# Kernel tuning notes

Hardware: AMD Instinct MI355X
Metric: run time of the kernel (lower is better)

## Reference

```python
import jax, jax.numpy as jnp
import numpy as np

# --- basis bookkeeping (mirrors TwoBodyToSpherical._generate_buffers) ---
METADATA = np.array([3, 2, 1], dtype=np.int64)          # shells per l
N_IRREPS = 2 * np.arange(3, dtype=np.int64) + 1          # 2l+1
REP_OFFSETS = np.concatenate([[0], np.cumsum(METADATA * N_IRREPS)[:-1]])
NUM_REPS_1D = int((METADATA * N_IRREPS).sum())           # = 14
M_IDX_MAP = {0: [0], 1: [0, 2, 1], 2: [0, 1, 2, 3, 4]}
ANGULAR = {"s": 0, "p": 1, "d": 2}

C_AOS = ["1s", "2s", "3s"] + ["2p"] * 3 + ["3p"] * 3 + ["3d"] * 5
H_AOS = ["1s", "2s"]


def _build_repid_map(aos):
    # faithful port of the per-element repid_map construction (valence_only=True)
    repid = np.zeros(len(aos), dtype=np.int64)
    dst_n, l_last, m_qc = 0, 0, 0
    for i, ao in enumerate(aos):
        l = ANGULAR[ao[1]]
        if l > l_last:
            dst_n = 0
        repid[i] = REP_OFFSETS[l] + dst_n + M_IDX_MAP[l][m_qc] * METADATA[l]
        if m_qc == 2 * l:
            m_qc = 0
            dst_n += 1
        else:
            m_qc += 1
        l_last = l
    return repid


def setup_inputs() -> dict:
    key = jax.random.key(0)
    maps = {"C": _build_repid_map(C_AOS), "H": _build_repid_map(H_AOS)}
    atomsybs = ["C"] * 400 + ["H"] * 100               # 500 atoms
    n_atoms = len(atomsybs)
    dst_rep_ids_1d = np.concatenate([maps[a] for a in atomsybs])
    lens = np.array([len(maps[a]) for a in atomsybs], dtype=np.int64)
    dst_offsets_1d = np.repeat(np.arange(n_atoms, dtype=np.int64), lens)
    dst_flat_ids_1d = dst_offsets_1d * NUM_REPS_1D + dst_rep_ids_1d  # [N_ao]=5800
    n_ao = dst_flat_ids_1d.shape[0]
    feat_ten = jax.random.normal(key, (n_ao, n_ao), dtype=jnp.float32)
    return {
        "feat_ten": feat_ten,
        "dst_flat_ids_1d": jnp.asarray(dst_flat_ids_1d, dtype=jnp.int32),
        "n_atoms": n_atoms,
        "num_reps_1d": NUM_REPS_1D,
    }


def reference(feat_ten, dst_flat_ids_1d, n_atoms, num_reps_1d):
    total = n_atoms * num_reps_1d                        # 7000
    # 2D destination flat ids: outer-sum of 1D ids (rep_dims=(0,1))
    ids2d = (dst_flat_ids_1d[:, None] * total + dst_flat_ids_1d[None, :]).reshape(-1)
    flat = feat_ten.reshape(-1)
    out_flat = jnp.zeros((total * total,), dtype=feat_ten.dtype).at[ids2d].add(flat)
    # view(n_atoms, R, n_atoms, R) then transpose(1,2) -> [A, A, R, R]
    out = out_flat.reshape(n_atoms, num_reps_1d, n_atoms, num_reps_1d)
    return jnp.transpose(out, (0, 2, 1, 3))
```

## Files before the change

kernel.cpp:

```cpp
#include <hip/hip_runtime.h>

constexpr int R = 14;
constexpr int A = 500;
constexpr int TOTAL = A * R;
constexpr int TILE = R * R;
constexpr int G = 25;
constexpr int NG = A / G;
constexpr int SUPER = 4;
constexpr int NSUP = NG / SUPER;
constexpr int WP = 356;
constexpr int CHUNK = G * TILE;

__global__ __launch_bounds__(1024) void setup_kernel(
        const int* __restrict__ dst, int n_ao,
        int* __restrict__ inv, int* __restrict__ arow,
        int* __restrict__ ncols, int* __restrict__ pm) {
    int tid = threadIdx.x;
    for (int t = tid; t < TOTAL; t += 1024) inv[t] = -1;
    __syncthreads();
    for (int t = tid; t < n_ao; t += 1024) inv[dst[t]] = t;
    __syncthreads();
    if (tid < A) {
        int a = tid, lo = 0x7fffffff, hi = -1;
#pragma unroll
        for (int r = 0; r < R; ++r) {
            int v = inv[a * R + r];
            if (v >= 0) { lo = min(lo, v); hi = max(hi, v); }
        }
        arow[a] = lo;
        ncols[a] = hi - lo + 1;
#pragma unroll
        for (int r = 0; r < R; ++r) {
            int v = inv[a * R + r];
            pm[a * R + r] = (v >= 0) ? (v - lo) : -1;
        }
    }
}

__global__ __launch_bounds__(512, 6) void tile_kernel(
        const float* __restrict__ feat,
        const int* __restrict__ arow,
        const int* __restrict__ ncols,
        const int* __restrict__ pm,
        float* __restrict__ out, int n_ao) {
    const int gs  = blockIdx.x % NSUP;
    const int a1  = blockIdx.x / NSUP;
    const int tid = threadIdx.x;

    __shared__ float buf[2][R][WP];
    __shared__ int s_pr[R];
    __shared__ int s_pc[SUPER][G * R];
    __shared__ int s_off[SUPER][G];
    __shared__ int s_colA[SUPER];
    __shared__ int s_W4[SUPER];

    const int arow1 = arow[a1];
    const int n1    = ncols[a1];
    const int gbase = gs * (SUPER * G);

    if (tid < R) s_pr[tid] = pm[a1 * R + tid];
    for (int t = tid; t < SUPER * G * R; t += 512)
        (&s_pc[0][0])[t] = pm[gbase * R + t];
    if (tid < SUPER) {
        const int g0 = gbase + tid * G;
        const int colA = arow[g0] & ~3;
        s_colA[tid] = colA;
        s_W4[tid]   = (arow[g0 + G - 1] + ncols[g0 + G - 1] - colA + 3) >> 2;
    }
    if (tid < SUPER * G) {
        const int sI = tid / G, i = tid - sI * G;
        const int g0 = gbase + sI * G;
        s_off[sI][i] = arow[g0 + i] - (arow[g0] & ~3);
    }
    __syncthreads();

    int a2i_[3], dk_[3][4], ci_[3][4];
    bool val_[3];
#pragma unroll
    for (int j = 0; j < 3; ++j) {
        const int o4 = tid * 4 + j * 2048;
        val_[j] = (o4 < CHUNK);
        const int o = val_[j] ? o4 : 0;
        int a2i = o / TILE;
        int e   = o - a2i * TILE;
        int r1  = e / R;
        int r2  = e - r1 * R;
        a2i_[j] = a2i;
#pragma unroll
        for (int k = 0; k < 4; ++k) {
            dk_[j][k] = s_pr[r1];
            ci_[j][k] = a2i * R + r2;
            if (++r2 == R) { r2 = 0; ++r1; }
        }
    }

    const int d0  = tid >> 7;
    const int c4  = tid & 127;
    const int rs4 = n_ao >> 2;
    const float4* feat4 = reinterpret_cast<const float4*>(feat);

    float4 rg[4];

    auto stage_load = [&](int s) {
        const int W4 = s_W4[s];
        if (c4 < W4) {
            const float4* src = feat4 + (long long)arow1 * rs4 + (s_colA[s] >> 2) + c4;
#pragma unroll
            for (int u = 0; u < 4; ++u) {
                const int d = d0 + u * 4;
                if (d < n1) rg[u] = src[(long long)d * rs4];
            }
        }
    };
    auto stage_write = [&](int nb, int s) {
        const int W4 = s_W4[s];
        if (c4 < W4) {
#pragma unroll
            for (int u = 0; u < 4; ++u) {
                const int d = d0 + u * 4;
                if (d < n1)
                    *reinterpret_cast<float4*>(&buf[nb][d][c4 << 2]) = rg[u];
            }
        }
    };

    stage_load(0);
    stage_write(0, 0);
    __syncthreads();

    int cb = 0;
    for (int s = 0; s < SUPER; ++s) {
        if (s + 1 < SUPER) stage_load(s + 1);

        const long long outbase =
            ((long long)a1 * A + gbase + s * G) * (long long)TILE;
        const int* pcS = &s_pc[s][0];
#pragma unroll
        for (int j = 0; j < 3; ++j) {
            if (!val_[j]) continue;
            const int off = s_off[s][a2i_[j]];
            float4 v;
            float* vp = &v.x;
#pragma unroll
            for (int k = 0; k < 4; ++k) {
                const int d = dk_[j][k];
                const int c = pcS[ci_[j][k]];
                vp[k] = ((d | c) >= 0) ? buf[cb][d][off + c] : 0.0f;
            }
            *reinterpret_cast<float4*>(out + outbase + tid * 4 + j * 2048) = v;
        }

        if (s + 1 < SUPER) {
            stage_write(cb ^ 1, s + 1);
            __syncthreads();
            cb ^= 1;
        }
    }
}

extern "C" void kernel_launch(void* const* d_in, const int* in_sizes, int n_in,
                              void* d_out, int out_size, void* d_ws, size_t ws_size,
                              hipStream_t stream) {
    const float* feat = (const float*)d_in[0];
    const int*   dst  = (const int*)d_in[1];
    int n_ao = in_sizes[1];

    int* inv   = (int*)d_ws;
    int* arow  = inv + TOTAL;
    int* ncols = arow + A;
    int* pm    = ncols + A;

    setup_kernel<<<1, 1024, 0, stream>>>(dst, n_ao, inv, arow, ncols, pm);
    tile_kernel<<<A * NSUP, 512, 0, stream>>>(feat, arow, ncols, pm,
                                              (float*)d_out, n_ao);
}
```

Measured before the change: 351.5 us.

## Single-buffer LDS staging with nontemporal loads/stores and sentinel-based index masking

Drops the double-buffered register/LDS pipeline for a single LDS buffer that is staged directly from global memory with nontemporal loads, adding a second barrier per stage. It also replaces the -1 masks with a large negative sentinel so a single index sum decides validity, moves stage metadata out of shared memory into per-thread recomputation, and raises the occupancy hint to 8 blocks. Output uses nontemporal stores. The aim is lower LDS and register use for higher occupancy plus less cache pollution from the streaming output, at the cost of losing load/compute overlap within a block.

```diff
diff --git a/kernel.cpp b/kernel.cpp
--- a/kernel.cpp
+++ b/kernel.cpp
@@ -8,8 +8,11 @@
 constexpr int NG = A / G;
 constexpr int SUPER = 4;
 constexpr int NSUP = NG / SUPER;
-constexpr int WP = 356;
+constexpr int WP = 364;
 constexpr int CHUNK = G * TILE;
+constexpr int SENT = (int)0xC0000000;
+
+typedef float v4f __attribute__((ext_vector_type(4)));
 
 __global__ __launch_bounds__(1024) void setup_kernel(
         const int* __restrict__ dst, int n_ao,
@@ -37,7 +40,7 @@
     }
 }
 
-__global__ __launch_bounds__(512, 6) void tile_kernel(
+__global__ __launch_bounds__(512, 8) void tile_kernel(
         const float* __restrict__ feat,
         const int* __restrict__ arow,
         const int* __restrict__ ncols,
@@ -47,34 +50,25 @@
     const int a1  = blockIdx.x / NSUP;
     const int tid = threadIdx.x;
 
-    __shared__ float buf[2][R][WP];
-    __shared__ int s_pr[R];
+    __shared__ float buf[R * WP];
     __shared__ int s_pc[SUPER][G * R];
     __shared__ int s_off[SUPER][G];
-    __shared__ int s_colA[SUPER];
-    __shared__ int s_W4[SUPER];
 
     const int arow1 = arow[a1];
     const int n1    = ncols[a1];
     const int gbase = gs * (SUPER * G);
 
-    if (tid < R) s_pr[tid] = pm[a1 * R + tid];
-    for (int t = tid; t < SUPER * G * R; t += 512)
-        (&s_pc[0][0])[t] = pm[gbase * R + t];
-    if (tid < SUPER) {
-        const int g0 = gbase + tid * G;
-        const int colA = arow[g0] & ~3;
-        s_colA[tid] = colA;
-        s_W4[tid]   = (arow[g0 + G - 1] + ncols[g0 + G - 1] - colA + 3) >> 2;
+    for (int t = tid; t < SUPER * G * R; t += 512) {
+        const int pmv = pm[gbase * R + t];
+        (&s_pc[0][0])[t] = (pmv >= 0) ? pmv : SENT;
     }
     if (tid < SUPER * G) {
         const int sI = tid / G, i = tid - sI * G;
         const int g0 = gbase + sI * G;
         s_off[sI][i] = arow[g0 + i] - (arow[g0] & ~3);
     }
-    __syncthreads();
 
-    int a2i_[3], dk_[3][4], ci_[3][4];
+    int rb_[3][4], ci_[3][4], a2i_[3];
     bool val_[3];
 #pragma unroll
     for (int j = 0; j < 3; ++j) {
@@ -88,7 +82,8 @@
         a2i_[j] = a2i;
 #pragma unroll
         for (int k = 0; k < 4; ++k) {
-            dk_[j][k] = s_pr[r1];
+            const int dd = pm[a1 * R + r1];
+            rb_[j][k] = (dd >= 0) ? dd * WP : SENT;
             ci_[j][k] = a2i * R + r2;
             if (++r2 == R) { r2 = 0; ++r1; }
         }
@@ -97,41 +92,25 @@
     const int d0  = tid >> 7;
     const int c4  = tid & 127;
     const int rs4 = n_ao >> 2;
-    const float4* feat4 = reinterpret_cast<const float4*>(feat);
 
-    float4 rg[4];
-
-    auto stage_load = [&](int s) {
-        const int W4 = s_W4[s];
+    auto stage = [&](int s) {
+        const int g0   = gbase + s * G;
+        const int colA = arow[g0] & ~3;
+        const int W4   = (arow[g0 + G - 1] + ncols[g0 + G - 1] - colA + 3) >> 2;
         if (c4 < W4) {
-            const float4* src = feat4 + (long long)arow1 * rs4 + (s_colA[s] >> 2) + c4;
-#pragma unroll
-            for (int u = 0; u < 4; ++u) {
-                const int d = d0 + u * 4;
-                if (d < n1) rg[u] = src[(long long)d * rs4];
-            }
-        }
-    };
-    auto stage_write = [&](int nb, int s) {
-        const int W4 = s_W4[s];
-        if (c4 < W4) {
+            const v4f* src = reinterpret_cast<const v4f*>(feat)
+                           + (long long)arow1 * rs4 + (colA >> 2) + c4;
 #pragma unroll
             for (int u = 0; u < 4; ++u) {
                 const int d = d0 + u * 4;
                 if (d < n1)
-                    *reinterpret_cast<float4*>(&buf[nb][d][c4 << 2]) = rg[u];
+                    *reinterpret_cast<v4f*>(&buf[d * WP + (c4 << 2)]) =
+                        __builtin_nontemporal_load(src + (long long)d * rs4);
             }
         }
     };
 
-    stage_load(0);
-    stage_write(0, 0);
-    __syncthreads();
-
-    int cb = 0;
-    for (int s = 0; s < SUPER; ++s) {
-        if (s + 1 < SUPER) stage_load(s + 1);
-
+    auto emit = [&](int s) {
         const long long outbase =
             ((long long)a1 * A + gbase + s * G) * (long long)TILE;
         const int* pcS = &s_pc[s][0];
@@ -139,21 +118,27 @@
         for (int j = 0; j < 3; ++j) {
             if (!val_[j]) continue;
             const int off = s_off[s][a2i_[j]];
-            float4 v;
-            float* vp = &v.x;
+            v4f v;
 #pragma unroll
             for (int k = 0; k < 4; ++k) {
-                const int d = dk_[j][k];
-                const int c = pcS[ci_[j][k]];
-                vp[k] = ((d | c) >= 0) ? buf[cb][d][off + c] : 0.0f;
+                const int c   = pcS[ci_[j][k]];
+                const int idx = rb_[j][k] + off + c;
+                const float x = buf[max(idx, 0)];
+                ((float*)&v)[k] = (idx >= 0) ? x : 0.0f;
             }
-            *reinterpret_cast<float4*>(out + outbase + tid * 4 + j * 2048) = v;
+            __builtin_nontemporal_store(
+                v, reinterpret_cast<v4f*>(out + outbase + tid * 4 + j * 2048));
         }
+    };
 
+    stage(0);
+    __syncthreads();
+    for (int s = 0; s < SUPER; ++s) {
+        emit(s);
         if (s + 1 < SUPER) {
-            stage_write(cb ^ 1, s + 1);
             __syncthreads();
-            cb ^= 1;
+            stage(s + 1);
+            __syncthreads();
         }
     }
 }
```

New measurement: 302.2 us. 1.16x faster.
